# Performance work log

Measured on AMD Instinct MI355X. Metric: run time of the kernel, lower is better.

The kernel has to match this reference:

```python
import jax, jax.numpy as jnp
import numpy as np

N_SPECIES = 119
N_RADIAL = 5
N_BASIS = 7
R_MIN = 0.5
R_MAX = 6.0
UNITS = (512, 512)
EMB_NORM = 1.0 / np.sqrt(N_BASIS)
N_ATOMS = 20000
N_PAIRS = 800000
N_FEAT = 360  # gaussian moments for n_radial=5, n_contr=8

# triangular index sets for symmetric contractions
_t2i, _t2j = np.tril_indices(N_RADIAL)  # 15 unique (r,s) pairs
_t3 = np.array([(i, j, k) for i in range(N_RADIAL) for j in range(i + 1) for k in range(j + 1)])
_t3i, _t3j, _t3k = _t3[:, 0], _t3[:, 1], _t3[:, 2]  # 35 unique (r,s,t) triples


def _forward(R, Z, neighbor, offsets, embeddings, W1, b1, W2, b2, W3, b3):
    n_atoms = R.shape[0]
    idx_i, idx_j = neighbor[0], neighbor[1]
    # --- distance computation (free space, init_box == 0) ---
    dr_vec = R[idx_j] - R[idx_i] + offsets                      # (P,3)
    dr = jnp.sqrt(jnp.sum(dr_vec * dr_vec, axis=-1))            # (P,)
    dn = dr_vec / (dr + 1e-5)[:, None]                          # unit vectors
    # --- gaussian radial basis + species-pair embedding + cosine cutoff ---
    shifts = jnp.linspace(R_MIN, R_MAX, N_BASIS)
    betta = N_BASIS ** 2 / R_MAX ** 2
    rad_norm = (2.0 * betta / np.pi) ** 0.75
    basis = rad_norm * jnp.exp(-betta * (dr[:, None] - shifts) ** 2)   # (P,B)
    cutoff = 0.5 * (jnp.cos(np.pi * dr / R_MAX) + 1.0) * (dr < R_MAX)
    emb = embeddings[Z[idx_j], Z[idx_i]]                               # (P,R,B)
    radial = EMB_NORM * jnp.einsum('prb,pb->pr', emb, basis) * cutoff[:, None]  # (P,R)
    # --- geometric moments, aggregated per central atom ---
    m1 = radial[:, :, None] * dn[:, None, :]                    # (P,R,3)
    m2 = m1[..., None] * dn[:, None, None, :]                   # (P,R,3,3)
    m3 = m2[..., None] * dn[:, None, None, None, :]             # (P,R,3,3,3)
    seg = lambda x: jax.ops.segment_sum(x, idx_i, num_segments=n_atoms)
    M0, M1, M2, M3 = seg(radial), seg(m1), seg(m2), seg(m3)
    # --- invariant contractions (gaussian moments) ---
    c1 = jnp.einsum('ari,asi->ars', M1, M1)[:, _t2i, _t2j]
    c2 = jnp.einsum('arij,asij->ars', M2, M2)[:, _t2i, _t2j]
    c3 = jnp.einsum('arijk,asijk->ars', M3, M3)[:, _t2i, _t2j]
    c4 = jnp.einsum('arij,asik,atjk->arst', M2, M2, M2)[:, _t3i, _t3j, _t3k]
    c5 = jnp.einsum('ari,asj,atij->arst', M1, M1, M2)[:, _t2i, _t2j].reshape(n_atoms, -1)
    c6 = jnp.einsum('arijk,asijl,atkl->arst', M3, M3, M2)[:, _t2i, _t2j].reshape(n_atoms, -1)
    c7 = jnp.einsum('arijk,asij,atk->arst', M3, M2, M1).reshape(n_atoms, -1)
    feats = jnp.concatenate([M0, c1, c2, c3, c4, c5, c6, c7], axis=-1)  # (A,360)
    # --- vmapped per-atom NTK readout MLP (swish) ---
    h = jax.nn.swish(feats @ W1 / np.sqrt(N_FEAT) + 0.1 * b1)
    h = jax.nn.swish(h @ W2 / np.sqrt(UNITS[0]) + 0.1 * b2)
    out = h @ W3 / np.sqrt(UNITS[1]) + 0.1 * b3                 # (A,1)
    # --- mask padded atoms (Z == 0) ---
    out = out * (Z > 0)[:, None]
    return out


def setup_inputs() -> dict:
    key = jax.random.key(0)
    ks = jax.random.split(key, 8)
    R = jax.random.uniform(ks[0], (N_ATOMS, 3), jnp.float32) * 12.0  # 12 A cube
    Z = jax.random.randint(ks[1], (N_ATOMS,), 0, N_SPECIES, jnp.int32)
    neighbor = jax.random.randint(ks[2], (2, N_PAIRS), 0, N_ATOMS, jnp.int32)
    # avoid degenerate self pairs (dr == 0 would NaN the unit vector grad)
    idx_i, idx_j = neighbor[0], neighbor[1]
    idx_j = jnp.where(idx_j == idx_i, (idx_j + 1) % N_ATOMS, idx_j)
    neighbor = jnp.stack([idx_i, idx_j], axis=0)
    box = jnp.zeros((3, 3), jnp.float32)
    offsets = jnp.zeros((N_PAIRS, 3), jnp.float32)
    embeddings = jax.random.normal(ks[3], (N_SPECIES, N_SPECIES, N_RADIAL, N_BASIS), jnp.float32)
    W1 = jax.random.normal(ks[4], (N_FEAT, UNITS[0]), jnp.float32)
    b1 = jnp.zeros((UNITS[0],), jnp.float32)
    W2 = jax.random.normal(ks[5], (UNITS[0], UNITS[1]), jnp.float32)
    b2 = jnp.zeros((UNITS[1],), jnp.float32)
    W3 = jax.random.normal(ks[6], (UNITS[1], 1), jnp.float32)
    b3 = jnp.zeros((1,), jnp.float32)
    return dict(R=R, Z=Z, neighbor=neighbor, box=box, offsets=offsets,
                embeddings=embeddings, W1=W1, b1=b1, W2=W2, b2=b2, W3=W3, b3=b3)


def reference(R, Z, neighbor, box, offsets, embeddings, W1, b1, W2, b2, W3, b3):
    # box is unused: init_box == 0 selects the free-space displacement fn
    return _forward(R, Z, neighbor, offsets, embeddings, W1, b1, W2, b2, W3, b3)
```

## Files before the change

kernel.cpp:

```cpp
#include <hip/hip_runtime.h>
#include <hip/hip_bf16.h>
#include <cmath>

#define NSP 119
#define UNITS 512
#define NFEAT 360
#define KP1 384

typedef __attribute__((ext_vector_type(8))) short short8;
typedef __attribute__((ext_vector_type(4))) float floatx4;

__device__ __host__ constexpr int s2c(int i, int j) {
    return (i > j) ? i*(i+1)/2 + j : j*(j+1)/2 + i;
}
__device__ __host__ constexpr int s3c(int x, int y, int z) {
    int A = x > y ? x : y; A = A > z ? A : z;
    int C = x < y ? x : y; C = C < z ? C : z;
    int B = x + y + z - A - C;
    return A*(A+1)*(A+2)/6 + B*(B+1)/2 + C;
}

struct BasisConsts {
    float f0k;
    float kg;
    float scale;
    float c[6];
};

__global__ __launch_bounds__(256) void prep_kernel(
    const float* __restrict__ W1, const float* __restrict__ W2,
    __hip_bfloat16* __restrict__ W1t, __hip_bfloat16* __restrict__ W2t,
    int* __restrict__ counts, float* __restrict__ outbuf, int natoms)
{
    int b = blockIdx.x;
    if (b < 448) {
        __shared__ float tile[32][33];
        const float* W; __hip_bfloat16* Wt; int K, Kp, ik, in;
        if (b < 192) { W = W1; Wt = W1t; K = NFEAT; Kp = KP1; ik = b % 12; in = b / 12; }
        else { int b2 = b - 192; W = W2; Wt = W2t; K = UNITS; Kp = UNITS; ik = b2 & 15; in = b2 >> 4; }
        int tx = threadIdx.x & 31, ty = threadIdx.x >> 5;
        int n = in * 32 + tx;
        #pragma unroll
        for (int pp = 0; pp < 4; ++pp) {
            int kk = ty + pp * 8;
            int k = ik * 32 + kk;
            tile[kk][tx] = (k < K) ? W[(size_t)k * UNITS + n] : 0.f;
        }
        __syncthreads();
        #pragma unroll
        for (int pp = 0; pp < 4; ++pp) {
            int nn = ty + pp * 8;
            Wt[(size_t)(in * 32 + nn) * Kp + ik * 32 + tx] = __float2bfloat16(tile[tx][nn]);
        }
    } else {
        int idx = (b - 448) * 256 + threadIdx.x;
        if (idx < natoms) { counts[idx] = 0; outbuf[idx] = 0.f; }
    }
}

__global__ __launch_bounds__(256) void hist_kernel(
    const float* __restrict__ R, const int* __restrict__ nbr,
    const float* __restrict__ offsets, int* __restrict__ counts, int npairs)
{
    int p = blockIdx.x * 256 + threadIdx.x;
    if (p >= npairs) return;
    int i = nbr[p];
    int j = nbr[npairs + p];
    float dx = R[3*j]   - R[3*i]   + offsets[3*p];
    float dy = R[3*j+1] - R[3*i+1] + offsets[3*p+1];
    float dz = R[3*j+2] - R[3*i+2] + offsets[3*p+2];
    float dr2 = fmaf(dz, dz, fmaf(dy, dy, dx*dx));
    if (dr2 < 36.0f) atomicAdd(&counts[i], 1);
}

__global__ __launch_bounds__(1024) void scan_kernel(
    const int* __restrict__ counts, int* __restrict__ offs,
    int* __restrict__ cursor, int n)
{
    int tid = threadIdx.x;
    int lane = tid & 63, wid = tid >> 6;
    int beg = tid * 32;
    int local[32];
    int s = 0;
    if (beg + 32 <= n) {
        int4 w[8];
        const int4* cp = (const int4*)(counts + beg);
        #pragma unroll
        for (int j = 0; j < 8; ++j) w[j] = cp[j];
        const int* wf = (const int*)w;
        #pragma unroll
        for (int k = 0; k < 32; ++k) { local[k] = s; s += wf[k]; }
    } else {
        #pragma unroll
        for (int k = 0; k < 32; ++k) {
            int idx = beg + k;
            int v = (idx < n) ? counts[idx] : 0;
            local[k] = s; s += v;
        }
    }
    int incl = s;
    #pragma unroll
    for (int off = 1; off < 64; off <<= 1) {
        int t = __shfl_up(incl, off, 64);
        if (lane >= off) incl += t;
    }
    __shared__ int wsum[16];
    if (lane == 63) wsum[wid] = incl;
    __syncthreads();
    if (tid < 16) {
        int v = wsum[tid];
        int inc2 = v;
        #pragma unroll
        for (int off = 1; off < 16; off <<= 1) {
            int t = __shfl_up(inc2, off, 64);
            if (tid >= off) inc2 += t;
        }
        wsum[tid] = inc2 - v;
    }
    __syncthreads();
    int base = wsum[wid] + (incl - s);
    if (beg + 32 <= n) {
        int4* op = (int4*)(offs + beg);
        int4* cp2 = (int4*)(cursor + beg);
        #pragma unroll
        for (int j = 0; j < 8; ++j) {
            int4 t;
            t.x = base + local[j*4];   t.y = base + local[j*4+1];
            t.z = base + local[j*4+2]; t.w = base + local[j*4+3];
            op[j] = t; cp2[j] = t;
        }
    } else {
        #pragma unroll
        for (int k = 0; k < 32; ++k) {
            int idx = beg + k;
            if (idx < n) { int v = base + local[k]; offs[idx] = v; cursor[idx] = v; }
        }
    }
}

__global__ __launch_bounds__(256) void scatter_pair_kernel(
    const float* __restrict__ R, const int* __restrict__ Z,
    const int* __restrict__ nbr, const float* __restrict__ offsets,
    const float* __restrict__ emb, int* __restrict__ cursor,
    float* __restrict__ pairdata, int npairs, BasisConsts bc)
{
    int p = blockIdx.x * 256 + threadIdx.x;
    if (p >= npairs) return;
    int i = nbr[p];
    int j = nbr[npairs + p];
    float dx = R[3*j]   - R[3*i]   + offsets[3*p];
    float dy = R[3*j+1] - R[3*i+1] + offsets[3*p+1];
    float dz = R[3*j+2] - R[3*i+2] + offsets[3*p+2];
    float dr2 = fmaf(dz, dz, fmaf(dy, dy, dx*dx));
    if (dr2 >= 36.0f) return;
    int pos = atomicAdd(&cursor[i], 1);

    float dr  = sqrtf(dr2);
    float inv = 1.0f / (dr + 1e-5f);
    float d0  = dr - 0.5f;
    float basis[7];
    basis[0] = exp2f(bc.f0k * d0 * d0);
    float G  = exp2f(bc.kg * dr);
    float cur = basis[0];
    #pragma unroll
    for (int b = 0; b < 6; ++b) { cur *= G * bc.c[b]; basis[b+1] = cur; }
    float cut = 0.5f * (__cosf(dr * 0.52359877559829887f) + 1.0f);
    float s = bc.scale * cut;

    const float* e = emb + ((size_t)Z[j] * NSP + Z[i]) * 35;
    float ev[35];
    __builtin_memcpy(ev, e, 35 * sizeof(float));

    float rec[8];
    #pragma unroll
    for (int r = 0; r < 5; ++r) {
        float acc = 0.f;
        #pragma unroll
        for (int b = 0; b < 7; ++b) acc += ev[r*7+b] * basis[b];
        rec[r] = s * acc;
    }
    rec[5] = dx * inv; rec[6] = dy * inv; rec[7] = dz * inv;
    float4* out = (float4*)(pairdata + (size_t)pos * 8);
    out[0] = make_float4(rec[0], rec[1], rec[2], rec[3]);
    out[1] = make_float4(rec[4], rec[5], rec[6], rec[7]);
}

#define SREC 28
__global__ __launch_bounds__(256) void moment_kernel(
    const float* __restrict__ pairdata, const int* __restrict__ offs,
    const int* __restrict__ counts, float* __restrict__ momG, int natoms)
{
    int wv = threadIdx.x >> 6, lane = threadIdx.x & 63;
    int a = blockIdx.x * 4 + wv;
    __shared__ float stage[4][64][SREC];

    int start = 0, cnt = 0;
    if (a < natoms) { start = offs[a]; cnt = counts[a]; }

    int cr0, pk0;
    if (lane < 5)       { cr0 = lane;            pk0 = 0; }
    else if (lane < 20) { int c = lane - 5;      cr0 = c / 3;  pk0 = 1 + c % 3; }
    else if (lane < 50) { int c = lane - 20;     cr0 = c / 6;  pk0 = 4 + c % 6; }
    else                { int c = lane - 50;     cr0 = c / 10; pk0 = 10 + c % 10; }
    int cr1 = 0, pk1 = 0;
    if (lane < 36) { int c = 14 + lane; cr1 = c / 10; pk1 = 10 + c % 10; }

    float acc0 = 0.f, acc1 = 0.f;
    for (int base = 0; base < cnt; base += 64) {
        int m = min(64, cnt - base);
        if (lane < m) {
            const float4* pd = (const float4*)(pairdata + (size_t)(start + base + lane) * 8);
            float4 u = pd[0], v = pd[1];
            float x = v.y, y = v.z, z = v.w;
            float s2_0 = x*x, s2_1 = y*x, s2_2 = y*y, s2_3 = z*x, s2_4 = z*y, s2_5 = z*z;
            float* st = stage[wv][lane];
            ((float4*)st)[0] = u;
            ((float4*)st)[1] = make_float4(v.x, 1.0f, x, y);
            ((float4*)st)[2] = make_float4(z, s2_0, s2_1, s2_2);
            ((float4*)st)[3] = make_float4(s2_3, s2_4, s2_5, s2_0*x);
            ((float4*)st)[4] = make_float4(s2_0*y, s2_2*x, s2_2*y, s2_0*z);
            ((float4*)st)[5] = make_float4(s2_1*z, s2_2*z, s2_5*x, s2_5*y);
            ((float4*)st)[6] = make_float4(s2_5*z, 0.f, 0.f, 0.f);
        }
        __builtin_amdgcn_wave_barrier();
        for (int q = 0; q < m; ++q) {
            const float* s = stage[wv][q];
            acc0 += s[cr0] * s[5 + pk0];
            acc1 += s[cr1] * s[5 + pk1];
        }
        __builtin_amdgcn_wave_barrier();
    }
    size_t base = (size_t)(a >> 6) * 6400 + (size_t)(a & 63);
    momG[base + (size_t)lane * 64] = acc0;
    if (lane < 36) momG[base + (size_t)(64 + lane) * 64] = acc1;
}

#define LROW 390
__global__ __launch_bounds__(256) void feat_kernel(
    const float* __restrict__ momG, __hip_bfloat16* __restrict__ feats)
{
    constexpr int cT2I[15] = {0,1,1,2,2,2,3,3,3,3,4,4,4,4,4};
    constexpr int cT2J[15] = {0,0,1,0,1,2,0,1,2,3,0,1,2,3,4};
    constexpr int cT3A[35] = {0, 1,1,1, 2,2,2,2,2,2, 3,3,3,3,3,3,3,3,3,3, 4,4,4,4,4,4,4,4,4,4,4,4,4,4,4};
    constexpr int cT3B[35] = {0, 0,1,1, 0,1,1,2,2,2, 0,1,1,2,2,2,3,3,3,3, 0,1,1,2,2,2,3,3,3,3,4,4,4,4,4};
    constexpr int cT3C[35] = {0, 0,0,1, 0,0,1,0,1,2, 0,0,1,0,1,2,0,1,2,3, 0,0,1,0,1,2,0,1,2,3,0,1,2,3,4};
    constexpr float cW2[6]  = {1.f,2.f,1.f,2.f,2.f,1.f};
    constexpr float cW3[10] = {1.f,3.f,3.f,1.f,3.f,6.f,3.f,3.f,3.f,1.f};

    __shared__ __hip_bfloat16 ldsF[64][LROW];
    int wv = threadIdx.x >> 6, lane = threadIdx.x & 63;
    const float* mg = momG + (size_t)blockIdx.x * 6400 + lane;

    #define LDM(e) mg[(e) * 64]
    #define STF(f, v) ldsF[lane][(f)] = __float2bfloat16(v)

    if (wv == 0) {
        float m3[50], m2[30];
        #pragma unroll
        for (int e = 0; e < 50; ++e) m3[e] = LDM(50 + e);
        #pragma unroll
        for (int e = 0; e < 30; ++e) m2[e] = LDM(20 + e);
        #pragma unroll
        for (int p = 0; p < 10; ++p) {
            int r = cT2I[p], s = cT2J[p];
            float B2v[9];
            #pragma unroll
            for (int z = 0; z < 3; ++z)
                #pragma unroll
                for (int w = 0; w < 3; ++w) {
                    float acc = 0.f;
                    #pragma unroll
                    for (int x = 0; x < 3; ++x)
                        #pragma unroll
                        for (int y = 0; y < 3; ++y)
                            acc += m3[r*10 + s3c(x,y,z)] * m3[s*10 + s3c(x,y,w)];
                    B2v[z*3+w] = acc;
                }
            #pragma unroll
            for (int t = 0; t < 5; ++t) {
                float acc = 0.f;
                #pragma unroll
                for (int z = 0; z < 3; ++z)
                    #pragma unroll
                    for (int w = 0; w < 3; ++w)
                        acc += B2v[z*3+w] * m2[t*6 + s2c(z,w)];
                STF(160 + p*5 + t, acc);
            }
        }
    } else if (wv == 1) {
        float m0[5], m1[15], m2[30];
        #pragma unroll
        for (int e = 0; e < 5; ++e)  m0[e] = LDM(e);
        #pragma unroll
        for (int e = 0; e < 15; ++e) m1[e] = LDM(5 + e);
        #pragma unroll
        for (int e = 0; e < 30; ++e) m2[e] = LDM(20 + e);
        #pragma unroll
        for (int r = 0; r < 5; ++r) STF(r, m0[r]);
        #pragma unroll
        for (int p = 0; p < 15; ++p) {
            int r = cT2I[p], s = cT2J[p];
            float v1 = m1[r*3]*m1[s*3] + m1[r*3+1]*m1[s*3+1] + m1[r*3+2]*m1[s*3+2];
            STF(5 + p, v1);
            float v2 = 0.f;
            #pragma unroll
            for (int k = 0; k < 6; ++k) v2 += cW2[k] * m2[r*6+k] * m2[s*6+k];
            STF(20 + p, v2);
        }
        #pragma unroll
        for (int q = 0; q < 35; ++q) {
            int r = cT3A[q], s = cT3B[q], t = cT3C[q];
            float v = 0.f;
            #pragma unroll
            for (int x = 0; x < 3; ++x)
                #pragma unroll
                for (int y = 0; y < 3; ++y) {
                    float d = 0.f;
                    #pragma unroll
                    for (int z = 0; z < 3; ++z)
                        d += m2[s*6 + s2c(x,z)] * m2[t*6 + s2c(y,z)];
                    v += m2[r*6 + s2c(x,y)] * d;
                }
            STF(50 + q, v);
        }
        #pragma unroll
        for (int f = NFEAT; f < KP1; ++f) STF(f, 0.f);
    } else if (wv == 2) {
        float m1[15], m2[30], m3[50];
        #pragma unroll
        for (int e = 0; e < 15; ++e) m1[e] = LDM(5 + e);
        #pragma unroll
        for (int e = 0; e < 30; ++e) m2[e] = LDM(20 + e);
        #pragma unroll
        for (int e = 0; e < 50; ++e) m3[e] = LDM(50 + e);
        #pragma unroll
        for (int p = 10; p < 15; ++p) {
            int r = cT2I[p], s = cT2J[p];
            float B2v[9];
            #pragma unroll
            for (int z = 0; z < 3; ++z)
                #pragma unroll
                for (int w = 0; w < 3; ++w) {
                    float acc = 0.f;
                    #pragma unroll
                    for (int x = 0; x < 3; ++x)
                        #pragma unroll
                        for (int y = 0; y < 3; ++y)
                            acc += m3[r*10 + s3c(x,y,z)] * m3[s*10 + s3c(x,y,w)];
                    B2v[z*3+w] = acc;
                }
            #pragma unroll
            for (int t = 0; t < 5; ++t) {
                float acc = 0.f;
                #pragma unroll
                for (int z = 0; z < 3; ++z)
                    #pragma unroll
                    for (int w = 0; w < 3; ++w)
                        acc += B2v[z*3+w] * m2[t*6 + s2c(z,w)];
                STF(160 + p*5 + t, acc);
            }
        }
        #pragma unroll
        for (int p = 0; p < 15; ++p) {
            int r = cT2I[p], s = cT2J[p];
            float o[9];
            #pragma unroll
            for (int x = 0; x < 3; ++x)
                #pragma unroll
                for (int y = 0; y < 3; ++y) o[x*3+y] = m1[r*3+x] * m1[s*3+y];
            #pragma unroll
            for (int t = 0; t < 5; ++t) {
                float v = 0.f;
                #pragma unroll
                for (int x = 0; x < 3; ++x)
                    #pragma unroll
                    for (int y = 0; y < 3; ++y)
                        v += o[x*3+y] * m2[t*6 + s2c(x,y)];
                STF(85 + p*5 + t, v);
            }
        }
    } else {
        float m1[15], m2[30], m3[50];
        #pragma unroll
        for (int e = 0; e < 15; ++e) m1[e] = LDM(5 + e);
        #pragma unroll
        for (int e = 0; e < 30; ++e) m2[e] = LDM(20 + e);
        #pragma unroll
        for (int e = 0; e < 50; ++e) m3[e] = LDM(50 + e);
        #pragma unroll
        for (int p = 0; p < 15; ++p) {
            int r = cT2I[p], s = cT2J[p];
            float v = 0.f;
            #pragma unroll
            for (int k = 0; k < 10; ++k) v += cW3[k] * m3[r*10+k] * m3[s*10+k];
            STF(35 + p, v);
        }
        #pragma unroll
        for (int r = 0; r < 5; ++r)
            #pragma unroll
            for (int s = 0; s < 5; ++s) {
                float A3z[3];
                #pragma unroll
                for (int z = 0; z < 3; ++z) {
                    float v = 0.f;
                    #pragma unroll
                    for (int x = 0; x < 3; ++x)
                        #pragma unroll
                        for (int y = 0; y < 3; ++y)
                            v += m3[r*10 + s3c(x,y,z)] * m2[s*6 + s2c(x,y)];
                    A3z[z] = v;
                }
                #pragma unroll
                for (int t = 0; t < 5; ++t) {
                    float v = A3z[0]*m1[t*3] + A3z[1]*m1[t*3+1] + A3z[2]*m1[t*3+2];
                    STF(235 + r*25 + s*5 + t, v);
                }
            }
    }
    __syncthreads();

    __hip_bfloat16* dst = feats + (size_t)blockIdx.x * 64 * KP1;
    #pragma unroll
    for (int rr = 0; rr < 16; ++rr) {
        int row = wv * 16 + rr;
        #pragma unroll
        for (int it = 0; it < 3; ++it) {
            uint32_t v = *(const uint32_t*)&ldsF[row][(it*64 + lane)*2];
            *(uint32_t*)&dst[(size_t)row * KP1 + (size_t)(it*64 + lane)*2] = v;
        }
    }
    #undef LDM
    #undef STF
}

__global__ __launch_bounds__(256) void gemm_mfma_swish(
    const __hip_bfloat16* __restrict__ A, const __hip_bfloat16* __restrict__ Bt,
    const float* __restrict__ bias, __hip_bfloat16* __restrict__ C,
    const float* __restrict__ w3, float* __restrict__ outacc,
    int Kp, int M, int Mtiles, float alpha, float a3, int fuse)
{
    __shared__ float4 As[2][512];
    __shared__ float4 Bs[2][512];
    int tid = threadIdx.x;
    int wave = tid >> 6, lane = tid & 63;
    int quad = lane >> 4, l16 = lane & 15;
    int wm = wave >> 1, wn = wave & 1;
    int bid = blockIdx.x;
    int mt = (bid >> 5) * 8 + (bid & 7);
    int nt = (bid >> 3) & 3;
    if (mt >= Mtiles) return;
    int rowBase = mt * 128;
    int colBase = nt * 128;

    floatx4 acc[4][4] = {};

    int rA0 = tid >> 2, cA = tid & 3;
    int rA1 = rA0 + 64;
    int pA0 = rA0 * 4 + (cA ^ ((rA0 >> 1) & 3));
    int pA1 = rA1 * 4 + (cA ^ ((rA1 >> 1) & 3));

    const char* pa0 = (const char*)(A  + (size_t)(rowBase + rA0) * Kp + cA * 8);
    const char* pa1 = (const char*)(A  + (size_t)(rowBase + rA1) * Kp + cA * 8);
    const char* pb0 = (const char*)(Bt + (size_t)(colBase + rA0) * Kp + cA * 8);
    const char* pb1 = (const char*)(Bt + (size_t)(colBase + rA1) * Kp + cA * 8);

    int posA[4], posB[4];
    #pragma unroll
    for (int t = 0; t < 4; ++t) {
        int rr = wm * 64 + t * 16 + l16;
        posA[t] = rr * 4 + (quad ^ ((rr >> 1) & 3));
    }
    #pragma unroll
    for (int u = 0; u < 4; ++u) {
        int cc = wn * 64 + u * 16 + l16;
        posB[u] = cc * 4 + (quad ^ ((cc >> 1) & 3));
    }

    int nK = Kp >> 5;
    float4 ra0 = *(const float4*)pa0;
    float4 ra1 = *(const float4*)pa1;
    float4 rb0 = *(const float4*)pb0;
    float4 rb1 = *(const float4*)pb1;

    for (int kt = 0; kt < nK; ++kt) {
        int buf = kt & 1;
        As[buf][pA0] = ra0;
        As[buf][pA1] = ra1;
        Bs[buf][pA0] = rb0;
        Bs[buf][pA1] = rb1;
        __syncthreads();
        if (kt + 1 < nK) {
            int off = (kt + 1) << 6;
            ra0 = *(const float4*)(pa0 + off);
            ra1 = *(const float4*)(pa1 + off);
            rb0 = *(const float4*)(pb0 + off);
            rb1 = *(const float4*)(pb1 + off);
        }
        short8 af[4], bf[4];
        #pragma unroll
        for (int t = 0; t < 4; ++t) af[t] = *(const short8*)(As[buf] + posA[t]);
        #pragma unroll
        for (int u = 0; u < 4; ++u) bf[u] = *(const short8*)(Bs[buf] + posB[u]);
        #pragma unroll
        for (int t = 0; t < 4; ++t)
            #pragma unroll
            for (int u = 0; u < 4; ++u)
                acc[t][u] = __builtin_amdgcn_mfma_f32_16x16x32_bf16(
                    af[t], bf[u], acc[t][u], 0, 0, 0);
    }

    if (!fuse) {
        #pragma unroll
        for (int u = 0; u < 4; ++u) {
            int col = colBase + wn * 64 + u * 16 + l16;
            float bc = 0.1f * bias[col];
            #pragma unroll
            for (int t = 0; t < 4; ++t) {
                int row0 = rowBase + wm * 64 + t * 16 + quad * 4;
                #pragma unroll
                for (int r = 0; r < 4; ++r) {
                    float x = alpha * acc[t][u][r] + bc;
                    float v = x / (1.f + expf(-x));
                    C[(size_t)(row0 + r) * UNITS + col] = __float2bfloat16(v);
                }
            }
        }
    } else {
        float rowsum[4][4] = {};
        #pragma unroll
        for (int u = 0; u < 4; ++u) {
            int col = colBase + wn * 64 + u * 16 + l16;
            float bc = 0.1f * bias[col];
            float w3c = w3[col] * a3;
            #pragma unroll
            for (int t = 0; t < 4; ++t)
                #pragma unroll
                for (int r = 0; r < 4; ++r) {
                    float x = alpha * acc[t][u][r] + bc;
                    float v = x / (1.f + expf(-x));
                    rowsum[t][r] += v * w3c;
                }
        }
        #pragma unroll
        for (int t = 0; t < 4; ++t)
            #pragma unroll
            for (int r = 0; r < 4; ++r) {
                float s = rowsum[t][r];
                s += __shfl_xor(s, 1, 64);
                s += __shfl_xor(s, 2, 64);
                s += __shfl_xor(s, 4, 64);
                s += __shfl_xor(s, 8, 64);
                rowsum[t][r] = s;
            }
        if (l16 == 0) {
            #pragma unroll
            for (int t = 0; t < 4; ++t) {
                int row0 = rowBase + wm * 64 + t * 16 + quad * 4;
                #pragma unroll
                for (int r = 0; r < 4; ++r)
                    if (row0 + r < M) atomicAdd(&outacc[row0 + r], rowsum[t][r]);
            }
        }
    }
}

__global__ void finalize_kernel(float* __restrict__ out, const int* __restrict__ Z,
                                const float* __restrict__ b3, int natoms)
{
    int a = blockIdx.x * 256 + threadIdx.x;
    if (a >= natoms) return;
    float v = out[a] + 0.1f * b3[0];
    out[a] = (Z[a] > 0) ? v : 0.f;
}

static inline size_t align_up(size_t x, size_t a) { return (x + a - 1) & ~(a - 1); }

extern "C" void kernel_launch(void* const* d_in, const int* in_sizes, int n_in,
                              void* d_out, int out_size, void* d_ws, size_t ws_size,
                              hipStream_t stream)
{
    const float* R       = (const float*)d_in[0];
    const int*   Z       = (const int*)  d_in[1];
    const int*   nbr     = (const int*)  d_in[2];
    const float* offsets = (const float*)d_in[4];
    const float* emb     = (const float*)d_in[5];
    const float* W1      = (const float*)d_in[6];
    const float* b1      = (const float*)d_in[7];
    const float* W2      = (const float*)d_in[8];
    const float* b2      = (const float*)d_in[9];
    const float* W3      = (const float*)d_in[10];
    const float* b3      = (const float*)d_in[11];

    int natoms = in_sizes[0] / 3;
    int npairs = in_sizes[2] / 2;
    int Mpad = ((natoms + 127) / 128) * 128;
    int Mtiles = Mpad / 128;

    char* ws = (char*)d_ws;
    size_t off = 0;
    int* counts = (int*)(ws + off); off = align_up(off + natoms*4, 256);
    int* offs   = (int*)(ws + off); off = align_up(off + natoms*4, 256);
    int* cursor = (int*)(ws + off); off = align_up(off + natoms*4, 256);
    float* pairdata = (float*)(ws + off); off = align_up(off + (size_t)npairs*8*4, 256);
    float* momG = (float*)(ws + off); off = align_up(off + (size_t)Mpad*100*4, 256);
    __hip_bfloat16* W1t   = (__hip_bfloat16*)(ws + off); off = align_up(off + (size_t)UNITS*KP1*2, 256);
    __hip_bfloat16* W2t   = (__hip_bfloat16*)(ws + off); off = align_up(off + (size_t)UNITS*UNITS*2, 256);
    __hip_bfloat16* feats = (__hip_bfloat16*)(ws + off); off = align_up(off + (size_t)Mpad*KP1*2, 256);
    __hip_bfloat16* h1    = (__hip_bfloat16*)(ws + off); off = align_up(off + (size_t)Mpad*UNITS*2, 256);

    BasisConsts bc;
    {
        const double betta = 49.0 / 36.0;
        const double delta = 5.5 / 6.0;
        const double log2e = 1.4426950408889634073599246810;
        bc.f0k = (float)(-betta * log2e);
        bc.kg  = (float)(2.0 * betta * delta * log2e);
        for (int b = 0; b < 6; ++b)
            bc.c[b] = (float)exp(-betta * delta * (1.0 + delta * (2*b + 1)));
        bc.scale = (float)(pow(2.0 * betta / M_PI, 0.75) / sqrt(7.0));
    }

    int prepBlocks = 448 + (natoms + 255) / 256;
    prep_kernel<<<dim3(prepBlocks), 256, 0, stream>>>(
        W1, W2, W1t, W2t, counts, (float*)d_out, natoms);

    int pgrid = (npairs + 255) / 256;
    hist_kernel<<<dim3(pgrid), 256, 0, stream>>>(R, nbr, offsets, counts, npairs);
    scan_kernel<<<dim3(1), 1024, 0, stream>>>(counts, offs, cursor, natoms);
    scatter_pair_kernel<<<dim3(pgrid), 256, 0, stream>>>(
        R, Z, nbr, offsets, emb, cursor, pairdata, npairs, bc);

    moment_kernel<<<dim3(Mpad / 4), 256, 0, stream>>>(
        pairdata, offs, counts, momG, natoms);
    feat_kernel<<<dim3(Mpad / 64), 256, 0, stream>>>(momG, feats);

    float a1 = 1.0f / sqrtf((float)NFEAT);
    float a2 = 1.0f / sqrtf((float)UNITS);
    int gemmGrid = ((Mtiles + 7) / 8) * 8 * 4;
    gemm_mfma_swish<<<dim3(gemmGrid), 256, 0, stream>>>(
        feats, W1t, b1, h1, nullptr, nullptr, KP1, natoms, Mtiles, a1, 0.f, 0);
    gemm_mfma_swish<<<dim3(gemmGrid), 256, 0, stream>>>(
        h1, W2t, b2, nullptr, W3, (float*)d_out, UNITS, natoms, Mtiles, a2, a2, 1);

    finalize_kernel<<<dim3((natoms + 255) / 256), 256, 0, stream>>>(
        (float*)d_out, Z, b3, natoms);
}
```

Measured before the change: 214.4 us.

## Compute pair records once with compacted append, sort indices instead of records

The separate histogram pass and the second full pair pass are merged into one pair kernel that evaluates each pair once. It appends records compactly using a wave-level ballot plus one global atomic per wave, and also counts pairs per atom. A small scatter kernel then builds a per-atom sorted index list, and the moment kernel gathers records indirectly through it. The finalize kernel is folded into the output initialization and the GEMM epilogue's species mask. This removes a redundant distance pass and a kernel launch, at the cost of an extra indirection and uncoalesced record reads in the moment kernel.

Result: slower. 350.9 us (+63.7%).

```diff
diff --git a/kernel.cpp b/kernel.cpp
--- a/kernel.cpp
+++ b/kernel.cpp
@@ -30,7 +30,9 @@
 __global__ __launch_bounds__(256) void prep_kernel(
     const float* __restrict__ W1, const float* __restrict__ W2,
     __hip_bfloat16* __restrict__ W1t, __hip_bfloat16* __restrict__ W2t,
-    int* __restrict__ counts, float* __restrict__ outbuf, int natoms)
+    int* __restrict__ counts, float* __restrict__ outbuf,
+    const int* __restrict__ Z, const float* __restrict__ b3,
+    int* __restrict__ gcount, int natoms)
 {
     int b = blockIdx.x;
     if (b < 448) {
@@ -54,106 +56,48 @@
         }
     } else {
         int idx = (b - 448) * 256 + threadIdx.x;
-        if (idx < natoms) { counts[idx] = 0; outbuf[idx] = 0.f; }
-    }
-}
-
-__global__ __launch_bounds__(256) void hist_kernel(
-    const float* __restrict__ R, const int* __restrict__ nbr,
-    const float* __restrict__ offsets, int* __restrict__ counts, int npairs)
-{
-    int p = blockIdx.x * 256 + threadIdx.x;
-    if (p >= npairs) return;
-    int i = nbr[p];
-    int j = nbr[npairs + p];
-    float dx = R[3*j]   - R[3*i]   + offsets[3*p];
-    float dy = R[3*j+1] - R[3*i+1] + offsets[3*p+1];
-    float dz = R[3*j+2] - R[3*i+2] + offsets[3*p+2];
-    float dr2 = fmaf(dz, dz, fmaf(dy, dy, dx*dx));
-    if (dr2 < 36.0f) atomicAdd(&counts[i], 1);
-}
-
-__global__ __launch_bounds__(1024) void scan_kernel(
-    const int* __restrict__ counts, int* __restrict__ offs,
-    int* __restrict__ cursor, int n)
-{
-    int tid = threadIdx.x;
-    int lane = tid & 63, wid = tid >> 6;
-    int beg = tid * 32;
-    int local[32];
-    int s = 0;
-    if (beg + 32 <= n) {
-        int4 w[8];
-        const int4* cp = (const int4*)(counts + beg);
-        #pragma unroll
-        for (int j = 0; j < 8; ++j) w[j] = cp[j];
-        const int* wf = (const int*)w;
-        #pragma unroll
-        for (int k = 0; k < 32; ++k) { local[k] = s; s += wf[k]; }
-    } else {
-        #pragma unroll
-        for (int k = 0; k < 32; ++k) {
-            int idx = beg + k;
-            int v = (idx < n) ? counts[idx] : 0;
-            local[k] = s; s += v;
-        }
-    }
-    int incl = s;
-    #pragma unroll
-    for (int off = 1; off < 64; off <<= 1) {
-        int t = __shfl_up(incl, off, 64);
-        if (lane >= off) incl += t;
-    }
-    __shared__ int wsum[16];
-    if (lane == 63) wsum[wid] = incl;
-    __syncthreads();
-    if (tid < 16) {
-        int v = wsum[tid];
-        int inc2 = v;
-        #pragma unroll
-        for (int off = 1; off < 16; off <<= 1) {
-            int t = __shfl_up(inc2, off, 64);
-            if (tid >= off) inc2 += t;
-        }
-        wsum[tid] = inc2 - v;
-    }
-    __syncthreads();
-    int base = wsum[wid] + (incl - s);
-    if (beg + 32 <= n) {
-        int4* op = (int4*)(offs + beg);
-        int4* cp2 = (int4*)(cursor + beg);
-        #pragma unroll
-        for (int j = 0; j < 8; ++j) {
-            int4 t;
-            t.x = base + local[j*4];   t.y = base + local[j*4+1];
-            t.z = base + local[j*4+2]; t.w = base + local[j*4+3];
-            op[j] = t; cp2[j] = t;
-        }
-    } else {
-        #pragma unroll
-        for (int k = 0; k < 32; ++k) {
-            int idx = beg + k;
-            if (idx < n) { int v = base + local[k]; offs[idx] = v; cursor[idx] = v; }
-        }
-    }
-}
-
-__global__ __launch_bounds__(256) void scatter_pair_kernel(
+        if (idx < natoms) {
+            counts[idx] = 0;
+            outbuf[idx] = (Z[idx] > 0) ? 0.1f * b3[0] : 0.f;
+        }
+        if (idx == 0) gcount[0] = 0;
+    }
+}
+
+__global__ __launch_bounds__(256) void pair_compute_kernel(
     const float* __restrict__ R, const int* __restrict__ Z,
     const int* __restrict__ nbr, const float* __restrict__ offsets,
-    const float* __restrict__ emb, int* __restrict__ cursor,
-    float* __restrict__ pairdata, int npairs, BasisConsts bc)
+    const float* __restrict__ emb, int* __restrict__ counts,
+    int* __restrict__ gcount, float* __restrict__ tmpRec,
+    int* __restrict__ tmpI, int npairs, BasisConsts bc)
 {
     int p = blockIdx.x * 256 + threadIdx.x;
-    if (p >= npairs) return;
-    int i = nbr[p];
-    int j = nbr[npairs + p];
-    float dx = R[3*j]   - R[3*i]   + offsets[3*p];
-    float dy = R[3*j+1] - R[3*i+1] + offsets[3*p+1];
-    float dz = R[3*j+2] - R[3*i+2] + offsets[3*p+2];
+    int lane = threadIdx.x & 63;
+    bool inr = p < npairs;
+    int i = 0, j = 0;
+    float dx = 0.f, dy = 0.f, dz = 0.f;
+    if (inr) {
+        i = nbr[p];
+        j = nbr[npairs + p];
+        dx = R[3*j]   - R[3*i]   + offsets[3*p];
+        dy = R[3*j+1] - R[3*i+1] + offsets[3*p+1];
+        dz = R[3*j+2] - R[3*i+2] + offsets[3*p+2];
+    }
     float dr2 = fmaf(dz, dz, fmaf(dy, dy, dx*dx));
-    if (dr2 >= 36.0f) return;
-    int pos = atomicAdd(&cursor[i], 1);
+    bool valid = inr && (dr2 < 36.0f);
+
+    unsigned long long mask = __ballot(valid);
+    if (mask == 0ull) return;
+    int cnt = __popcll(mask);
+    int prefix = __popcll(mask & ((1ull << lane) - 1ull));
+    int leader = __ffsll((unsigned long long)mask) - 1;
+    int base = 0;
+    if (lane == leader) base = atomicAdd(gcount, cnt);
+    base = __shfl(base, leader, 64);
+    if (!valid) return;
+    int pos = base + prefix;
+
+    atomicAdd(&counts[i], 1);
 
     float dr  = sqrtf(dr2);
     float inv = 1.0f / (dr + 1e-5f);
@@ -180,15 +124,93 @@
         rec[r] = s * acc;
     }
     rec[5] = dx * inv; rec[6] = dy * inv; rec[7] = dz * inv;
-    float4* out = (float4*)(pairdata + (size_t)pos * 8);
+    tmpI[pos] = i;
+    float4* out = (float4*)(tmpRec + (size_t)pos * 8);
     out[0] = make_float4(rec[0], rec[1], rec[2], rec[3]);
     out[1] = make_float4(rec[4], rec[5], rec[6], rec[7]);
 }
 
+__global__ __launch_bounds__(1024) void scan_kernel(
+    const int* __restrict__ counts, int* __restrict__ offs,
+    int* __restrict__ cursor, int n)
+{
+    int tid = threadIdx.x;
+    int lane = tid & 63, wid = tid >> 6;
+    int beg = tid * 32;
+    int local[32];
+    int s = 0;
+    if (beg + 32 <= n) {
+        int4 w[8];
+        const int4* cp = (const int4*)(counts + beg);
+        #pragma unroll
+        for (int j = 0; j < 8; ++j) w[j] = cp[j];
+        const int* wf = (const int*)w;
+        #pragma unroll
+        for (int k = 0; k < 32; ++k) { local[k] = s; s += wf[k]; }
+    } else {
+        #pragma unroll
+        for (int k = 0; k < 32; ++k) {
+            int idx = beg + k;
+            int v = (idx < n) ? counts[idx] : 0;
+            local[k] = s; s += v;
+        }
+    }
+    int incl = s;
+    #pragma unroll
+    for (int off = 1; off < 64; off <<= 1) {
+        int t = __shfl_up(incl, off, 64);
+        if (lane >= off) incl += t;
+    }
+    __shared__ int wsum[16];
+    if (lane == 63) wsum[wid] = incl;
+    __syncthreads();
+    if (tid < 16) {
+        int v = wsum[tid];
+        int inc2 = v;
+        #pragma unroll
+        for (int off = 1; off < 16; off <<= 1) {
+            int t = __shfl_up(inc2, off, 64);
+            if (tid >= off) inc2 += t;
+        }
+        wsum[tid] = inc2 - v;
+    }
+    __syncthreads();
+    int base = wsum[wid] + (incl - s);
+    if (beg + 32 <= n) {
+        int4* op = (int4*)(offs + beg);
+        int4* cp2 = (int4*)(cursor + beg);
+        #pragma unroll
+        for (int j = 0; j < 8; ++j) {
+            int4 t;
+            t.x = base + local[j*4];   t.y = base + local[j*4+1];
+            t.z = base + local[j*4+2]; t.w = base + local[j*4+3];
+            op[j] = t; cp2[j] = t;
+        }
+    } else {
+        #pragma unroll
+        for (int k = 0; k < 32; ++k) {
+            int idx = beg + k;
+            if (idx < n) { int v = base + local[k]; offs[idx] = v; cursor[idx] = v; }
+        }
+    }
+}
+
+__global__ __launch_bounds__(256) void scatter_idx_kernel(
+    const int* __restrict__ tmpI, const int* __restrict__ gcount,
+    int* __restrict__ cursor, int* __restrict__ sorted)
+{
+    int t = blockIdx.x * 256 + threadIdx.x;
+    if (t >= *gcount) return;
+    int i = tmpI[t];
+    int pos = atomicAdd(&cursor[i], 1);
+    sorted[pos] = t;
+}
+
 #define SREC 28
 __global__ __launch_bounds__(256) void moment_kernel(
-    const float* __restrict__ pairdata, const int* __restrict__ offs,
-    const int* __restrict__ counts, float* __restrict__ momG, int natoms)
+    const float* __restrict__ tmpRec, const int* __restrict__ sorted,
+    const int* __restrict__ offs, const int* __restrict__ counts,
+    float* __restrict__ momG, int natoms)
 {
     int wv = threadIdx.x >> 6, lane = threadIdx.x & 63;
     int a = blockIdx.x * 4 + wv;
@@ -209,7 +231,8 @@
     for (int base = 0; base < cnt; base += 64) {
         int m = min(64, cnt - base);
         if (lane < m) {
-            const float4* pd = (const float4*)(pairdata + (size_t)(start + base + lane) * 8);
+            int t = sorted[start + base + lane];
+            const float4* pd = (const float4*)(tmpRec + (size_t)t * 8);
             float4 u = pd[0], v = pd[1];
             float x = v.y, y = v.z, z = v.w;
             float s2_0 = x*x, s2_1 = y*x, s2_2 = y*y, s2_3 = z*x, s2_4 = z*y, s2_5 = z*z;
@@ -437,6 +460,7 @@
     const __hip_bfloat16* __restrict__ A, const __hip_bfloat16* __restrict__ Bt,
     const float* __restrict__ bias, __hip_bfloat16* __restrict__ C,
     const float* __restrict__ w3, float* __restrict__ outacc,
+    const int* __restrict__ Zmask,
     int Kp, int M, int Mtiles, float alpha, float a3, int fuse)
 {
     __shared__ float4 As[2][512];
@@ -557,20 +581,14 @@
             for (int t = 0; t < 4; ++t) {
                 int row0 = rowBase + wm * 64 + t * 16 + quad * 4;
                 #pragma unroll
-                for (int r = 0; r < 4; ++r)
-                    if (row0 + r < M) atomicAdd(&outacc[row0 + r], rowsum[t][r]);
+                for (int r = 0; r < 4; ++r) {
+                    int row = row0 + r;
+                    if (row < M && Zmask[row] > 0)
+                        atomicAdd(&outacc[row], rowsum[t][r]);
+                }
             }
         }
     }
-}
-
-__global__ void finalize_kernel(float* __restrict__ out, const int* __restrict__ Z,
-                                const float* __restrict__ b3, int natoms)
-{
-    int a = blockIdx.x * 256 + threadIdx.x;
-    if (a >= natoms) return;
-    float v = out[a] + 0.1f * b3[0];
-    out[a] = (Z[a] > 0) ? v : 0.f;
 }
 
 static inline size_t align_up(size_t x, size_t a) { return (x + a - 1) & ~(a - 1); }
@@ -601,7 +619,10 @@
     int* counts = (int*)(ws + off); off = align_up(off + natoms*4, 256);
     int* offs   = (int*)(ws + off); off = align_up(off + natoms*4, 256);
     int* cursor = (int*)(ws + off); off = align_up(off + natoms*4, 256);
-    float* pairdata = (float*)(ws + off); off = align_up(off + (size_t)npairs*8*4, 256);
+    int* gcount = (int*)(ws + off); off = align_up(off + 4, 256);
+    int* tmpI   = (int*)(ws + off); off = align_up(off + (size_t)npairs*4, 256);
+    int* sorted = (int*)(ws + off); off = align_up(off + (size_t)npairs*4, 256);
+    float* tmpRec = (float*)(ws + off); off = align_up(off + (size_t)npairs*8*4, 256);
     float* momG = (float*)(ws + off); off = align_up(off + (size_t)Mpad*100*4, 256);
     __hip_bfloat16* W1t   = (__hip_bfloat16*)(ws + off); off = align_up(off + (size_t)UNITS*KP1*2, 256);
     __hip_bfloat16* W2t   = (__hip_bfloat16*)(ws + off); off = align_up(off + (size_t)UNITS*UNITS*2, 256);
@@ -622,26 +643,23 @@
 
     int prepBlocks = 448 + (natoms + 255) / 256;
     prep_kernel<<<dim3(prepBlocks), 256, 0, stream>>>(
-        W1, W2, W1t, W2t, counts, (float*)d_out, natoms);
+        W1, W2, W1t, W2t, counts, (float*)d_out, Z, b3, gcount, natoms);
 
     int pgrid = (npairs + 255) / 256;
-    hist_kernel<<<dim3(pgrid), 256, 0, stream>>>(R, nbr, offsets, counts, npairs);
+    pair_compute_kernel<<<dim3(pgrid), 256, 0, stream>>>(
+        R, Z, nbr, offsets, emb, counts, gcount, tmpRec, tmpI, npairs, bc);
     scan_kernel<<<dim3(1), 1024, 0, stream>>>(counts, offs, cursor, natoms);
-    scatter_pair_kernel<<<dim3(pgrid), 256, 0, stream>>>(
-        R, Z, nbr, offsets, emb, cursor, pairdata, npairs, bc);
+    scatter_idx_kernel<<<dim3(pgrid), 256, 0, stream>>>(tmpI, gcount, cursor, sorted);
 
     moment_kernel<<<dim3(Mpad / 4), 256, 0, stream>>>(
-        pairdata, offs, counts, momG, natoms);
+        tmpRec, sorted, offs, counts, momG, natoms);
     feat_kernel<<<dim3(Mpad / 64), 256, 0, stream>>>(momG, feats);
 
     float a1 = 1.0f / sqrtf((float)NFEAT);
     float a2 = 1.0f / sqrtf((float)UNITS);
     int gemmGrid = ((Mtiles + 7) / 8) * 8 * 4;
     gemm_mfma_swish<<<dim3(gemmGrid), 256, 0, stream>>>(
-        feats, W1t, b1, h1, nullptr, nullptr, KP1, natoms, Mtiles, a1, 0.f, 0);
+        feats, W1t, b1, h1, nullptr, nullptr, nullptr, KP1, natoms, Mtiles, a1, 0.f, 0);
     gemm_mfma_swish<<<dim3(gemmGrid), 256, 0, stream>>>(
-        h1, W2t, b2, nullptr, W3, (float*)d_out, UNITS, natoms, Mtiles, a2, a2, 1);
-
-    finalize_kernel<<<dim3((natoms + 255) / 256), 256, 0, stream>>>(
-        (float*)d_out, Z, b3, natoms);
-}
+        h1, W2t, b2, nullptr, W3, (float*)d_out, Z, UNITS, natoms, Mtiles, a2, a2, 1);
+}
```
